# Kernel optimization log

Measured on AMD Instinct MI355X. Metric: run time of the kernel, lower is better.

The kernel has to match this reference:

```python
import jax, jax.numpy as jnp
import numpy as np

B, T, C = 256, 256, 384
HEADS = 6
HEAD_DIM = C // HEADS
WINDOW = 64


def setup_inputs() -> dict:
    key = jax.random.key(0)
    ks = jax.random.split(key, 5)
    scale = 0.02
    return {
        "x": jax.random.normal(ks[0], (B, T, C), dtype=jnp.float32),
        "qkv_w": jax.random.normal(ks[1], (C, 3 * C), dtype=jnp.float32) * scale,
        "qkv_b": jax.random.normal(ks[2], (3 * C,), dtype=jnp.float32) * scale,
        "proj_w": jax.random.normal(ks[3], (C, C), dtype=jnp.float32) * scale,
        "proj_b": jax.random.normal(ks[4], (C,), dtype=jnp.float32) * scale,
        "gate": jnp.ones((C,), dtype=jnp.float32),
    }


def reference(x, qkv_w, qkv_b, proj_w, proj_b, gate):
    Bx, Tx, Cx = x.shape
    qkv = x @ qkv_w + qkv_b                     # [B, T, 3C]
    q, k, v = jnp.split(qkv, 3, axis=-1)
    # [B, T, H, hd] -> [B, H, T, hd]
    q = q.reshape(Bx, Tx, HEADS, HEAD_DIM).transpose(0, 2, 1, 3)
    k = k.reshape(Bx, Tx, HEADS, HEAD_DIM).transpose(0, 2, 1, 3)
    v = v.reshape(Bx, Tx, HEADS, HEAD_DIM).transpose(0, 2, 1, 3)

    att = jnp.einsum("bhqd,bhkd->bhqk", q, k) * (1.0 / np.sqrt(HEAD_DIM).astype(np.float32))
    idx = jnp.arange(Tx)
    causal = idx[:, None] >= idx[None, :]                 # j <= i
    local = jnp.abs(idx[:, None] - idx[None, :]) <= WINDOW
    mask = (causal & local)[None, None, :, :]             # [1,1,T,T]
    att = jnp.where(mask, att, -jnp.inf)
    att = jax.nn.softmax(att, axis=-1)

    out = jnp.einsum("bhqk,bhkd->bhqd", att, v)           # [B, H, T, hd]
    out = out.transpose(0, 2, 1, 3).reshape(Bx, Tx, Cx)
    return (out * gate) @ proj_w + proj_b
```

## Files before the change

### kernel.cpp

```cpp
#include <hip/hip_runtime.h>
#include <hip/hip_bf16.h>

typedef unsigned short u16;
typedef __attribute__((ext_vector_type(8))) short short8;
typedef __attribute__((ext_vector_type(8))) unsigned short ushort8;
typedef __attribute__((ext_vector_type(4))) float f32x4;
typedef __attribute__((ext_vector_type(4))) float f4;

#define GLB_CAST(p) ((const __attribute__((address_space(1))) unsigned int*)(p))
#define LDS_CAST(p) ((__attribute__((address_space(3))) unsigned int*)(p))

__device__ __forceinline__ void gl_lds16(const void* g, void* l) {
  __builtin_amdgcn_global_load_lds(GLB_CAST(g), LDS_CAST(l), 16, 0, 0);
}

__device__ __forceinline__ u16 f2bf(float f) {
  __hip_bfloat16 b = __float2bfloat16(f);
  return __builtin_bit_cast(u16, b);
}

__global__ void transpose_cvt_k(const float* __restrict__ in,
                                u16* __restrict__ out, int R, int C) {
  __shared__ float tile[32][33];
  int c0 = blockIdx.x * 32, r0 = blockIdx.y * 32;
  int tx = threadIdx.x, ty = threadIdx.y;
#pragma unroll
  for (int i = 0; i < 32; i += 8)
    tile[ty + i][tx] = in[(size_t)(r0 + ty + i) * C + c0 + tx];
  __syncthreads();
#pragma unroll
  for (int i = 0; i < 32; i += 8)
    out[(size_t)(c0 + ty + i) * R + r0 + tx] = f2bf(tile[tx][ty + i]);
}

template <int EPI>
__global__ __launch_bounds__(256, 2) void gemm_k(
    const void* __restrict__ Av, const u16* __restrict__ Bt,
    const float* __restrict__ bias,
    u16* __restrict__ oQ, u16* __restrict__ oK, u16* __restrict__ oV,
    float* __restrict__ oF) {
  constexpr int K = 384;
  constexpr int NT = (EPI == 1) ? 9 : 3;
  __shared__ u16 As[64 * 384];
  __shared__ u16 Bs[4][3][1024];
  __shared__ float bias_s[NT * 128];

  const int tid = threadIdx.x;
  const int m0 = blockIdx.x * 64;
  const int lane = tid & 63, wid = tid >> 6;
  const int lo = lane & 15, hi = lane >> 4;
  const int wc = wid;

  for (int i = tid; i < NT * 128; i += 256) bias_s[i] = bias[i];

  const int bcol = wc * 32 + (lane >> 2);
  const int bc = ((lane & 3) ^ ((lane >> 3) & 3)) * 8;
  char* const slot_l = (char*)&Bs[0][0][0] + wid * 6144 + lane * 16;
  auto stageB = [&](int slot, int tn, int kt) {
    const u16* s = Bt + (size_t)(tn * 128 + bcol) * K + kt * 32 + bc;
    char* d = slot_l + slot * 2048;
    gl_lds16(s, d);
    gl_lds16(s + 16 * K, d + 1024);
  };

  stageB(0, 0, 0);
  stageB(1, 0, 1);

  if (EPI == 1) {
    const float* X = (const float*)Av;
#pragma unroll
    for (int i = 0; i < 12; ++i) {
      int c = tid + i * 256;
      int row = c / 48, cc = c % 48;
      const float* src = X + (size_t)(m0 + row) * K + cc * 8;
      f4 a = *(const f4*)src;
      f4 b = *(const f4*)(src + 4);
      ushort8 o;
#pragma unroll
      for (int j = 0; j < 4; ++j) { o[j] = f2bf(a[j]); o[4 + j] = f2bf(b[j]); }
      *(ushort8*)((char*)As + row * 768 + ((cc * 16) ^ ((row & 7) << 4))) = o;
    }
  } else {
    const u16* Ab = (const u16*)Av;
#pragma unroll
    for (int i = 0; i < 12; ++i) {
      int c = tid + i * 256;
      int row = c / 48, cc = c % 48;
      int cs = cc ^ (row & 7);
      gl_lds16(Ab + (size_t)(m0 + row) * K + cs * 8, (char*)As + c * 16);
    }
  }
  __syncthreads();

  const int akey = (lo & 7) << 4;
  const int rk = ((lo >> 1) & 3) << 4;
  int abase[4];
#pragma unroll
  for (int m = 0; m < 4; ++m) abase[m] = (m * 16 + lo) * 768;
  const int bbase = lo * 64 + (hi * 16 ^ rk);
  const char* const Asc = (const char*)As;
  const char* const sb0 = (const char*)&Bs[0][0][0] + wid * 6144;

  int rp[4][4];
#pragma unroll
  for (int m = 0; m < 4; ++m)
#pragma unroll
    for (int rr = 0; rr < 4; ++rr) {
      int gm = m0 + m * 16 + hi * 4 + rr;
      rp[m][rr] = (EPI == 1) ? ((gm >> 8) * 98304 + (gm & 255) * 64)
                             : gm * 384;
    }

  const f32x4 Z4 = {0.f, 0.f, 0.f, 0.f};

  for (int t = 0; t < NT; ++t) {
    f32x4 acc[4][2];
#pragma unroll
    for (int m = 0; m < 4; ++m) { acc[m][0] = Z4; acc[m][1] = Z4; }

#pragma unroll
    for (int kt = 0; kt < 12; ++kt) {
      if (kt == 0) asm volatile("s_waitcnt vmcnt(4)" ::: "memory");
      else         asm volatile("s_waitcnt vmcnt(2)" ::: "memory");

      const char* sb = sb0 + (kt % 3) * 2048;
      short8 af[4], bf[2];
#pragma unroll
      for (int m = 0; m < 4; ++m)
        af[m] = *(const short8*)(Asc + abase[m] + ((kt * 64 + hi * 16) ^ akey));
      bf[0] = *(const short8*)(sb + bbase);
      bf[1] = *(const short8*)(sb + 1024 + bbase);

      if (kt < 10)           stageB((kt + 2) % 3, t, kt + 2);
      else if (t + 1 < NT)   stageB((kt + 2) % 3, t + 1, kt - 10);

      __builtin_amdgcn_s_setprio(1);
#pragma unroll
      for (int m = 0; m < 4; ++m) {
        acc[m][0] = __builtin_amdgcn_mfma_f32_16x16x32_bf16(af[m], bf[0], acc[m][0], 0, 0, 0);
        acc[m][1] = __builtin_amdgcn_mfma_f32_16x16x32_bf16(af[m], bf[1], acc[m][1], 0, 0, 0);
      }
      __builtin_amdgcn_s_setprio(0);
    }

    float bs0 = bias_s[t * 128 + wc * 32 + lo];
    float bs1 = bias_s[t * 128 + wc * 32 + 16 + lo];
    if (EPI == 1) {
      int r3 = t / 3;
      u16* dst = (r3 == 0) ? oQ : ((r3 == 1) ? oK : oV);
      int hc0 = (t - r3 * 3) * 128 + wc * 32 + lo;
      int cp0 = ((hc0 >> 6) << 14) + (hc0 & 63);
      int hc1 = hc0 + 16;
      int cp1 = ((hc1 >> 6) << 14) + (hc1 & 63);
#pragma unroll
      for (int m = 0; m < 4; ++m)
#pragma unroll
        for (int rr = 0; rr < 4; ++rr) {
          dst[(size_t)(rp[m][rr] + cp0)] = f2bf(acc[m][0][rr] + bs0);
          dst[(size_t)(rp[m][rr] + cp1)] = f2bf(acc[m][1][rr] + bs1);
        }
    } else {
      int colb = t * 128 + wc * 32 + lo;
#pragma unroll
      for (int m = 0; m < 4; ++m)
#pragma unroll
        for (int rr = 0; rr < 4; ++rr) {
          oF[(size_t)(rp[m][rr] + colb)] = acc[m][0][rr] + bs0;
          oF[(size_t)(rp[m][rr] + colb + 16)] = acc[m][1][rr] + bs1;
        }
    }
  }
}

__global__ __launch_bounds__(256) void attn_k(
    const u16* __restrict__ Qb, const u16* __restrict__ Kb,
    const u16* __restrict__ Vb, const float* __restrict__ gate,
    u16* __restrict__ Ao) {
  __shared__ u16 Ks[128 * 64];
  __shared__ u16 Vs[64 * 128];
  __shared__ u16 Ps[4][16 * 128];
  const int bx = blockIdx.x;
  const int qt = bx & 3, bh = bx >> 2;
  const int h = bh % 6, b = bh / 6;
  const int i0 = qt * 64, j0 = i0 - 64;
  const int tid = threadIdx.x, w = tid >> 6, lane = tid & 63;
  const int lo = lane & 15, hi = lane >> 4;

  const u16* Kh = Kb + (size_t)bh * (256 * 64);
  const u16* Vh = Vb + (size_t)bh * (256 * 64);
  const u16* Qh = Qb + (size_t)bh * (256 * 64);

#pragma unroll
  for (int it = 0; it < 4; ++it) {
    int chunk = tid + it * 256;
    int row = chunk >> 3, cc = chunk & 7;
    int csrc = cc ^ (row & 7);
    int j = j0 + row; if (j < 0) j = 0;
    gl_lds16(Kh + j * 64 + csrc * 8, Ks + chunk * 8);
  }
#pragma unroll
  for (int it = 0; it < 4; ++it) {
    int c = tid + it * 256;
    int dc = c >> 7;
    int j = c & 127;
    int jj = j0 + j; if (jj < 0) jj = 0;
    ushort8 v = *(const ushort8*)(Vh + jj * 64 + dc * 8);
#pragma unroll
    for (int e = 0; e < 8; ++e) {
      int d = dc * 8 + e;
      *(u16*)((char*)Vs + ((d * 256 + 2 * j) ^ ((d & 7) << 4))) = v[e];
    }
  }

  const int iq = i0 + w * 16 + lo;
  short8 aq0 = *(const short8*)(Qh + iq * 64 + hi * 8);
  short8 aq1 = *(const short8*)(Qh + iq * 64 + 32 + hi * 8);

  __syncthreads();

  const f32x4 Z4 = {0.f, 0.f, 0.f, 0.f};
  f32x4 accS[8];
#pragma unroll
  for (int t = 0; t < 8; ++t) accS[t] = Z4;
#pragma unroll
  for (int t = 0; t < 8; ++t) {
    int key = t * 16 + lo;
    int base = key * 128;
    int sw = (key & 7) << 4;
    short8 bk0 = *(const short8*)((const char*)Ks + ((base + hi * 16) ^ sw));
    short8 bk1 = *(const short8*)((const char*)Ks + ((base + 64 + hi * 16) ^ sw));
    accS[t] = __builtin_amdgcn_mfma_f32_16x16x32_bf16(aq0, bk0, accS[t], 0, 0, 0);
    accS[t] = __builtin_amdgcn_mfma_f32_16x16x32_bf16(aq1, bk1, accS[t], 0, 0, 0);
  }

  float pv[4][8];
  float rinv[4];
#pragma unroll
  for (int r = 0; r < 4; ++r) {
    int i = i0 + w * 16 + hi * 4 + r;
    float mx = -1e30f;
    float vals[8];
#pragma unroll
    for (int t = 0; t < 8; ++t) {
      int j = j0 + t * 16 + lo;
      float s = accS[t][r] * 0.125f;
      bool ok = (j >= 0) && (j <= i) && (j >= i - 64);
      vals[t] = ok ? s : -1e30f;
      mx = fmaxf(mx, vals[t]);
    }
#pragma unroll
    for (int off = 1; off < 16; off <<= 1) mx = fmaxf(mx, __shfl_xor(mx, off));
    float sum = 0.f;
#pragma unroll
    for (int t = 0; t < 8; ++t) {
      float p = __expf(vals[t] - mx);
      pv[r][t] = p;
      sum += p;
    }
#pragma unroll
    for (int off = 1; off < 16; off <<= 1) sum += __shfl_xor(sum, off);
    rinv[r] = 1.0f / sum;
  }

  u16* Pw = Ps[w];
#pragma unroll
  for (int r = 0; r < 4; ++r) {
    int ql = hi * 4 + r;
    int sw = (ql & 7) << 4;
#pragma unroll
    for (int t = 0; t < 8; ++t) {
      int off = (ql * 256 + (t * 16 + lo) * 2) ^ sw;
      *(u16*)((char*)Pw + off) = f2bf(pv[r][t]);
    }
  }

  f32x4 accO[4];
#pragma unroll
  for (int dt = 0; dt < 4; ++dt) accO[dt] = Z4;
#pragma unroll
  for (int ks = 0; ks < 4; ++ks) {
    int offA = (lo * 256 + ks * 64 + hi * 16) ^ ((lo & 7) << 4);
    short8 ap = *(const short8*)((const char*)Pw + offA);
#pragma unroll
    for (int dt = 0; dt < 4; ++dt) {
      int d = dt * 16 + lo;
      int offB = (d * 256 + ks * 64 + hi * 16) ^ ((d & 7) << 4);
      short8 bv = *(const short8*)((const char*)Vs + offB);
      accO[dt] = __builtin_amdgcn_mfma_f32_16x16x32_bf16(ap, bv, accO[dt], 0, 0, 0);
    }
  }

#pragma unroll
  for (int dt = 0; dt < 4; ++dt) {
    int d = dt * 16 + lo;
    float gg = gate[h * 64 + d];
#pragma unroll
    for (int r = 0; r < 4; ++r) {
      int i = i0 + w * 16 + hi * 4 + r;
      float v = accO[dt][r] * rinv[r] * gg;
      Ao[(size_t)(b * 256 + i) * 384 + h * 64 + d] = f2bf(v);
    }
  }
}

extern "C" void kernel_launch(void* const* d_in, const int* in_sizes, int n_in,
                              void* d_out, int out_size, void* d_ws, size_t ws_size,
                              hipStream_t stream) {
  const float* x      = (const float*)d_in[0];
  const float* qkv_w  = (const float*)d_in[1];
  const float* qkv_b  = (const float*)d_in[2];
  const float* proj_w = (const float*)d_in[3];
  const float* proj_b = (const float*)d_in[4];
  const float* gate   = (const float*)d_in[5];
  float* out = (float*)d_out;

  char* ws = (char*)d_ws;
  u16* att  = (u16*)ws;
  u16* vbuf = (u16*)(ws + 50331648);
  u16* w1T  = (u16*)(ws + 100663296);
  u16* pT   = (u16*)(ws + 101548032);
  u16* qbuf = (u16*)d_out;
  u16* kbuf = (u16*)((char*)d_out + 50331648);

  transpose_cvt_k<<<dim3(1152 / 32, 384 / 32), dim3(32, 8), 0, stream>>>(qkv_w, w1T, 384, 1152);
  transpose_cvt_k<<<dim3(384 / 32, 384 / 32), dim3(32, 8), 0, stream>>>(proj_w, pT, 384, 384);

  gemm_k<1><<<1024, 256, 0, stream>>>(x, w1T, qkv_b, qbuf, kbuf, vbuf, nullptr);
  attn_k<<<256 * 6 * 4, 256, 0, stream>>>(qbuf, kbuf, vbuf, gate, att);
  gemm_k<2><<<1024, 256, 0, stream>>>(att, pT, proj_b, nullptr, nullptr, nullptr, out);
}
```

Before: 195.2 us.

## Use 2-wave GEMM blocks with 64x64 per-wave tiles

Both GEMM kernels drop from four waves per block to two, and each wave now computes a 64x64 output tile (4x4 MFMA accumulators) instead of 64x32. This doubles register-level reuse of the A fragments and cuts the LDS reads per MFMA. The cross-tile B prefetch is moved out of the k-loop to after the epilogue, which adds a vmcnt(0) drain on the last k step and leaves that load exposed. Fewer waves per block and launch bounds of (128,1) lower occupancy and latency hiding, while the larger accumulator set raises register pressure.

After: 213.6 us. +9.5%, slower.

```diff
diff --git a/kernel.cpp b/kernel.cpp
--- a/kernel.cpp
+++ b/kernel.cpp
@@ -34,7 +34,7 @@
 }
 
 template <int EPI>
-__global__ __launch_bounds__(256, 2) void gemm_k(
+__global__ __launch_bounds__(128, 1) void gemm_k(
     const void* __restrict__ Av, const u16* __restrict__ Bt,
     const float* __restrict__ bias,
     u16* __restrict__ oQ, u16* __restrict__ oK, u16* __restrict__ oV,
@@ -42,7 +42,7 @@
   constexpr int K = 384;
   constexpr int NT = (EPI == 1) ? 9 : 3;
   __shared__ u16 As[64 * 384];
-  __shared__ u16 Bs[4][3][1024];
+  __shared__ u16 Bs[2][3][2048];
   __shared__ float bias_s[NT * 128];
 
   const int tid = threadIdx.x;
@@ -51,16 +51,17 @@
   const int lo = lane & 15, hi = lane >> 4;
   const int wc = wid;
 
-  for (int i = tid; i < NT * 128; i += 256) bias_s[i] = bias[i];
-
-  const int bcol = wc * 32 + (lane >> 2);
-  const int bc = ((lane & 3) ^ ((lane >> 3) & 3)) * 8;
-  char* const slot_l = (char*)&Bs[0][0][0] + wid * 6144 + lane * 16;
+  for (int i = tid; i < NT * 128; i += 128) bias_s[i] = bias[i];
+
+  const int bcolo = wc * 64 + (lane >> 2);
+  const int bko = ((lane & 3) ^ ((lane >> 3) & 3)) * 8;
+  char* const slot_l = (char*)&Bs[0][0][0] + wid * 12288 + lane * 16;
   auto stageB = [&](int slot, int tn, int kt) {
-    const u16* s = Bt + (size_t)(tn * 128 + bcol) * K + kt * 32 + bc;
-    char* d = slot_l + slot * 2048;
-    gl_lds16(s, d);
-    gl_lds16(s + 16 * K, d + 1024);
+    const u16* s = Bt + (size_t)(tn * 128 + bcolo) * K + kt * 32 + bko;
+    char* d = slot_l + slot * 4096;
+#pragma unroll
+    for (int j = 0; j < 4; ++j)
+      gl_lds16(s + (size_t)(j * 16) * K, d + j * 1024);
   };
 
   stageB(0, 0, 0);
@@ -69,8 +70,8 @@
   if (EPI == 1) {
     const float* X = (const float*)Av;
 #pragma unroll
-    for (int i = 0; i < 12; ++i) {
-      int c = tid + i * 256;
+    for (int i = 0; i < 24; ++i) {
+      int c = tid + i * 128;
       int row = c / 48, cc = c % 48;
       const float* src = X + (size_t)(m0 + row) * K + cc * 8;
       f4 a = *(const f4*)src;
@@ -83,8 +84,8 @@
   } else {
     const u16* Ab = (const u16*)Av;
 #pragma unroll
-    for (int i = 0; i < 12; ++i) {
-      int c = tid + i * 256;
+    for (int i = 0; i < 24; ++i) {
+      int c = tid + i * 128;
       int row = c / 48, cc = c % 48;
       int cs = cc ^ (row & 7);
       gl_lds16(Ab + (size_t)(m0 + row) * K + cs * 8, (char*)As + c * 16);
@@ -99,7 +100,7 @@
   for (int m = 0; m < 4; ++m) abase[m] = (m * 16 + lo) * 768;
   const int bbase = lo * 64 + (hi * 16 ^ rk);
   const char* const Asc = (const char*)As;
-  const char* const sb0 = (const char*)&Bs[0][0][0] + wid * 6144;
+  const char* const sb0 = (const char*)&Bs[0][0][0] + wid * 12288;
 
   int rp[4][4];
 #pragma unroll
@@ -114,60 +115,68 @@
   const f32x4 Z4 = {0.f, 0.f, 0.f, 0.f};
 
   for (int t = 0; t < NT; ++t) {
-    f32x4 acc[4][2];
-#pragma unroll
-    for (int m = 0; m < 4; ++m) { acc[m][0] = Z4; acc[m][1] = Z4; }
+    f32x4 acc[4][4];
+#pragma unroll
+    for (int m = 0; m < 4; ++m)
+#pragma unroll
+      for (int n = 0; n < 4; ++n) acc[m][n] = Z4;
 
 #pragma unroll
     for (int kt = 0; kt < 12; ++kt) {
-      if (kt == 0) asm volatile("s_waitcnt vmcnt(4)" ::: "memory");
-      else         asm volatile("s_waitcnt vmcnt(2)" ::: "memory");
-
-      const char* sb = sb0 + (kt % 3) * 2048;
-      short8 af[4], bf[2];
+      if (kt == 11) asm volatile("s_waitcnt vmcnt(0)" ::: "memory");
+      else          asm volatile("s_waitcnt vmcnt(4)" ::: "memory");
+
+      const char* sb = sb0 + (kt % 3) * 4096;
+      short8 af[4], bf[4];
 #pragma unroll
       for (int m = 0; m < 4; ++m)
         af[m] = *(const short8*)(Asc + abase[m] + ((kt * 64 + hi * 16) ^ akey));
-      bf[0] = *(const short8*)(sb + bbase);
-      bf[1] = *(const short8*)(sb + 1024 + bbase);
-
-      if (kt < 10)           stageB((kt + 2) % 3, t, kt + 2);
-      else if (t + 1 < NT)   stageB((kt + 2) % 3, t + 1, kt - 10);
+#pragma unroll
+      for (int n = 0; n < 4; ++n)
+        bf[n] = *(const short8*)(sb + n * 1024 + bbase);
+
+      if (kt < 10) stageB((kt + 2) % 3, t, kt + 2);
 
       __builtin_amdgcn_s_setprio(1);
 #pragma unroll
-      for (int m = 0; m < 4; ++m) {
-        acc[m][0] = __builtin_amdgcn_mfma_f32_16x16x32_bf16(af[m], bf[0], acc[m][0], 0, 0, 0);
-        acc[m][1] = __builtin_amdgcn_mfma_f32_16x16x32_bf16(af[m], bf[1], acc[m][1], 0, 0, 0);
-      }
+      for (int m = 0; m < 4; ++m)
+#pragma unroll
+        for (int n = 0; n < 4; ++n)
+          acc[m][n] = __builtin_amdgcn_mfma_f32_16x16x32_bf16(af[m], bf[n], acc[m][n], 0, 0, 0);
       __builtin_amdgcn_s_setprio(0);
     }
 
-    float bs0 = bias_s[t * 128 + wc * 32 + lo];
-    float bs1 = bias_s[t * 128 + wc * 32 + 16 + lo];
     if (EPI == 1) {
       int r3 = t / 3;
       u16* dst = (r3 == 0) ? oQ : ((r3 == 1) ? oK : oV);
-      int hc0 = (t - r3 * 3) * 128 + wc * 32 + lo;
-      int cp0 = ((hc0 >> 6) << 14) + (hc0 & 63);
-      int hc1 = hc0 + 16;
-      int cp1 = ((hc1 >> 6) << 14) + (hc1 & 63);
-#pragma unroll
-      for (int m = 0; m < 4; ++m)
-#pragma unroll
-        for (int rr = 0; rr < 4; ++rr) {
-          dst[(size_t)(rp[m][rr] + cp0)] = f2bf(acc[m][0][rr] + bs0);
-          dst[(size_t)(rp[m][rr] + cp1)] = f2bf(acc[m][1][rr] + bs1);
-        }
+#pragma unroll
+      for (int n = 0; n < 4; ++n) {
+        int c = wc * 64 + n * 16 + lo;
+        int hc = (t - r3 * 3) * 128 + c;
+        int cp = ((hc >> 6) << 14) + (hc & 63);
+        float bs = bias_s[t * 128 + c];
+#pragma unroll
+        for (int m = 0; m < 4; ++m)
+#pragma unroll
+          for (int rr = 0; rr < 4; ++rr)
+            dst[(size_t)(rp[m][rr] + cp)] = f2bf(acc[m][n][rr] + bs);
+      }
     } else {
-      int colb = t * 128 + wc * 32 + lo;
-#pragma unroll
-      for (int m = 0; m < 4; ++m)
-#pragma unroll
-        for (int rr = 0; rr < 4; ++rr) {
-          oF[(size_t)(rp[m][rr] + colb)] = acc[m][0][rr] + bs0;
-          oF[(size_t)(rp[m][rr] + colb + 16)] = acc[m][1][rr] + bs1;
-        }
+#pragma unroll
+      for (int n = 0; n < 4; ++n) {
+        int col = t * 128 + wc * 64 + n * 16 + lo;
+        float bs = bias_s[col];
+#pragma unroll
+        for (int m = 0; m < 4; ++m)
+#pragma unroll
+          for (int rr = 0; rr < 4; ++rr)
+            oF[(size_t)(rp[m][rr] + col)] = acc[m][n][rr] + bs;
+      }
+    }
+
+    if (t + 1 < NT) {
+      stageB(0, t + 1, 0);
+      stageB(1, t + 1, 1);
     }
   }
 }
@@ -325,7 +334,7 @@
   transpose_cvt_k<<<dim3(1152 / 32, 384 / 32), dim3(32, 8), 0, stream>>>(qkv_w, w1T, 384, 1152);
   transpose_cvt_k<<<dim3(384 / 32, 384 / 32), dim3(32, 8), 0, stream>>>(proj_w, pT, 384, 384);
 
-  gemm_k<1><<<1024, 256, 0, stream>>>(x, w1T, qkv_b, qbuf, kbuf, vbuf, nullptr);
+  gemm_k<1><<<1024, 128, 0, stream>>>(x, w1T, qkv_b, qbuf, kbuf, vbuf, nullptr);
   attn_k<<<256 * 6 * 4, 256, 0, stream>>>(qbuf, kbuf, vbuf, gate, att);
-  gemm_k<2><<<1024, 256, 0, stream>>>(att, pT, proj_b, nullptr, nullptr, nullptr, out);
-}
+  gemm_k<2><<<1024, 128, 0, stream>>>(att, pT, proj_b, nullptr, nullptr, nullptr, out);
+}
```

## Write V transposed from QKV GEMM and stage epilogue through LDS for vector stores

Applied to the files above, without the earlier changes.

The QKV GEMM epilogue now packs each wave's accumulator tile through a small LDS scratch buffer so it can issue 16-byte vector stores for Q and K. V is written directly in a [head][dim][token] transposed layout. The attention kernel can then load V into LDS with async global-to-LDS copies instead of scalar transposing stores. The bias is now held in LDS as bf16, which rounds it slightly, and the extra LDS round trip adds work to the epilogue.

After: 189.8 us. 1.03x faster.

```diff
diff --git a/kernel.cpp b/kernel.cpp
--- a/kernel.cpp
+++ b/kernel.cpp
@@ -18,6 +18,10 @@
   __hip_bfloat16 b = __float2bfloat16(f);
   return __builtin_bit_cast(u16, b);
 }
+__device__ __forceinline__ float bf2f(u16 u) {
+  unsigned int x = ((unsigned int)u) << 16;
+  return __builtin_bit_cast(float, x);
+}
 
 __global__ void transpose_cvt_k(const float* __restrict__ in,
                                 u16* __restrict__ out, int R, int C) {
@@ -37,13 +41,14 @@
 __global__ __launch_bounds__(256, 2) void gemm_k(
     const void* __restrict__ Av, const u16* __restrict__ Bt,
     const float* __restrict__ bias,
-    u16* __restrict__ oQ, u16* __restrict__ oK, u16* __restrict__ oV,
+    u16* __restrict__ oQ, u16* __restrict__ oK, u16* __restrict__ oVT,
     float* __restrict__ oF) {
   constexpr int K = 384;
   constexpr int NT = (EPI == 1) ? 9 : 3;
   __shared__ u16 As[64 * 384];
   __shared__ u16 Bs[4][3][1024];
-  __shared__ float bias_s[NT * 128];
+  __shared__ u16 Rs[4][512];
+  __shared__ u16 bias_sh[NT * 128];
 
   const int tid = threadIdx.x;
   const int m0 = blockIdx.x * 64;
@@ -51,7 +56,7 @@
   const int lo = lane & 15, hi = lane >> 4;
   const int wc = wid;
 
-  for (int i = tid; i < NT * 128; i += 256) bias_s[i] = bias[i];
+  for (int i = tid; i < NT * 128; i += 256) bias_sh[i] = f2bf(bias[i]);
 
   const int bcol = wc * 32 + (lane >> 2);
   const int bc = ((lane & 3) ^ ((lane >> 3) & 3)) * 8;
@@ -100,16 +105,7 @@
   const int bbase = lo * 64 + (hi * 16 ^ rk);
   const char* const Asc = (const char*)As;
   const char* const sb0 = (const char*)&Bs[0][0][0] + wid * 6144;
-
-  int rp[4][4];
-#pragma unroll
-  for (int m = 0; m < 4; ++m)
-#pragma unroll
-    for (int rr = 0; rr < 4; ++rr) {
-      int gm = m0 + m * 16 + hi * 4 + rr;
-      rp[m][rr] = (EPI == 1) ? ((gm >> 8) * 98304 + (gm & 255) * 64)
-                             : gm * 384;
-    }
+  char* const rp_ = (char*)&Rs[0][0] + wid * 1024;
 
   const f32x4 Z4 = {0.f, 0.f, 0.f, 0.f};
 
@@ -143,30 +139,54 @@
       __builtin_amdgcn_s_setprio(0);
     }
 
-    float bs0 = bias_s[t * 128 + wc * 32 + lo];
-    float bs1 = bias_s[t * 128 + wc * 32 + 16 + lo];
+    float bs0 = bf2f(bias_sh[t * 128 + wc * 32 + lo]);
+    float bs1 = bf2f(bias_sh[t * 128 + wc * 32 + 16 + lo]);
+
     if (EPI == 1) {
-      int r3 = t / 3;
-      u16* dst = (r3 == 0) ? oQ : ((r3 == 1) ? oK : oV);
-      int hc0 = (t - r3 * 3) * 128 + wc * 32 + lo;
-      int cp0 = ((hc0 >> 6) << 14) + (hc0 & 63);
-      int hc1 = hc0 + 16;
-      int cp1 = ((hc1 >> 6) << 14) + (hc1 & 63);
+      const int r3 = t / 3;
+      u16* dst = (r3 == 0) ? oQ : ((r3 == 1) ? oK : oVT);
+      const int hcb = (t - r3 * 3) * 128 + wc * 32;
+      if (r3 < 2) {
+#pragma unroll
+        for (int p = 0; p < 4; ++p) {
+#pragma unroll
+          for (int n = 0; n < 2; ++n)
+#pragma unroll
+            for (int rr = 0; rr < 4; ++rr)
+              *(u16*)(rp_ + (hi * 4 + rr) * 64 + (n * 16 + lo) * 2) =
+                  f2bf(acc[p][n][rr] + (n ? bs1 : bs0));
+          ushort8 v = *(const ushort8*)(rp_ + (lane >> 2) * 64 + (lane & 3) * 16);
+          int hc = hcb + (lane & 3) * 8;
+          int gm = m0 + p * 16 + (lane >> 2);
+          dst += 0;
+          *(ushort8*)(dst + (((size_t)((gm >> 8) * 6 + (hc >> 6))) << 14) +
+                      (gm & 255) * 64 + (hc & 63)) = v;
+        }
+      } else {
+#pragma unroll
+        for (int p = 0; p < 4; ++p) {
+#pragma unroll
+          for (int n = 0; n < 2; ++n)
+#pragma unroll
+            for (int rr = 0; rr < 4; ++rr)
+              *(u16*)(rp_ + (n * 16 + lo) * 32 + (hi * 4 + rr) * 2) =
+                  f2bf(acc[p][n][rr] + (n ? bs1 : bs0));
+          ushort8 v = *(const ushort8*)(rp_ + (lane >> 1) * 32 + (lane & 1) * 16);
+          int hc = hcb + (lane >> 1);
+          int tg = (m0 & 255) + p * 16 + (lane & 1) * 8;
+          *(ushort8*)(dst + (((size_t)((m0 >> 8) * 6 + (hc >> 6))) << 14) +
+                      (hc & 63) * 256 + tg) = v;
+        }
+      }
+    } else {
+      const int colb = t * 128 + wc * 32 + lo;
 #pragma unroll
       for (int m = 0; m < 4; ++m)
 #pragma unroll
         for (int rr = 0; rr < 4; ++rr) {
-          dst[(size_t)(rp[m][rr] + cp0)] = f2bf(acc[m][0][rr] + bs0);
-          dst[(size_t)(rp[m][rr] + cp1)] = f2bf(acc[m][1][rr] + bs1);
-        }
-    } else {
-      int colb = t * 128 + wc * 32 + lo;
-#pragma unroll
-      for (int m = 0; m < 4; ++m)
-#pragma unroll
-        for (int rr = 0; rr < 4; ++rr) {
-          oF[(size_t)(rp[m][rr] + colb)] = acc[m][0][rr] + bs0;
-          oF[(size_t)(rp[m][rr] + colb + 16)] = acc[m][1][rr] + bs1;
+          int gm = m0 + m * 16 + hi * 4 + rr;
+          oF[(size_t)gm * 384 + colb] = acc[m][0][rr] + bs0;
+          oF[(size_t)gm * 384 + colb + 16] = acc[m][1][rr] + bs1;
         }
     }
   }
@@ -174,7 +194,7 @@
 
 __global__ __launch_bounds__(256) void attn_k(
     const u16* __restrict__ Qb, const u16* __restrict__ Kb,
-    const u16* __restrict__ Vb, const float* __restrict__ gate,
+    const u16* __restrict__ VTb, const float* __restrict__ gate,
     u16* __restrict__ Ao) {
   __shared__ u16 Ks[128 * 64];
   __shared__ u16 Vs[64 * 128];
@@ -187,7 +207,7 @@
   const int lo = lane & 15, hi = lane >> 4;
 
   const u16* Kh = Kb + (size_t)bh * (256 * 64);
-  const u16* Vh = Vb + (size_t)bh * (256 * 64);
+  const u16* Vh = VTb + (size_t)bh * (64 * 256);
   const u16* Qh = Qb + (size_t)bh * (256 * 64);
 
 #pragma unroll
@@ -200,16 +220,11 @@
   }
 #pragma unroll
   for (int it = 0; it < 4; ++it) {
-    int c = tid + it * 256;
-    int dc = c >> 7;
-    int j = c & 127;
-    int jj = j0 + j; if (jj < 0) jj = 0;
-    ushort8 v = *(const ushort8*)(Vh + jj * 64 + dc * 8);
-#pragma unroll
-    for (int e = 0; e < 8; ++e) {
-      int d = dc * 8 + e;
-      *(u16*)((char*)Vs + ((d * 256 + 2 * j) ^ ((d & 7) << 4))) = v[e];
-    }
+    int chunk = tid + it * 256;
+    int d = chunk >> 4, kc = chunk & 15;
+    int ksrc = kc ^ (d & 7);
+    int j = j0 + ksrc * 8; if (j < 0) j = 0;
+    gl_lds16(Vh + d * 256 + j, Vs + chunk * 8);
   }
 
   const int iq = i0 + w * 16 + lo;
@@ -316,7 +331,7 @@
 
   char* ws = (char*)d_ws;
   u16* att  = (u16*)ws;
-  u16* vbuf = (u16*)(ws + 50331648);
+  u16* vT   = (u16*)(ws + 50331648);
   u16* w1T  = (u16*)(ws + 100663296);
   u16* pT   = (u16*)(ws + 101548032);
   u16* qbuf = (u16*)d_out;
@@ -325,7 +340,7 @@
   transpose_cvt_k<<<dim3(1152 / 32, 384 / 32), dim3(32, 8), 0, stream>>>(qkv_w, w1T, 384, 1152);
   transpose_cvt_k<<<dim3(384 / 32, 384 / 32), dim3(32, 8), 0, stream>>>(proj_w, pT, 384, 384);
 
-  gemm_k<1><<<1024, 256, 0, stream>>>(x, w1T, qkv_b, qbuf, kbuf, vbuf, nullptr);
-  attn_k<<<256 * 6 * 4, 256, 0, stream>>>(qbuf, kbuf, vbuf, gate, att);
+  gemm_k<1><<<1024, 256, 0, stream>>>(x, w1T, qkv_b, qbuf, kbuf, vT, nullptr);
+  attn_k<<<256 * 6 * 4, 256, 0, stream>>>(qbuf, kbuf, vT, gate, att);
   gemm_k<2><<<1024, 256, 0, stream>>>(att, pT, proj_b, nullptr, nullptr, nullptr, out);
 }
```
